# Kernel optimization log

Measured on AMD Instinct MI355X. Metric: run time of the kernel, lower is better.

Reference implementation:

```python
import jax, jax.numpy as jnp
import numpy as np

N_IN, N_REC, T, BATCH = 128, 512, 1000, 64
ALPHA = 0.2
SIGMA = float(np.sqrt(2.0 / ALPHA) * 0.05)  # sqrt(2/alpha)*sigma_rec
EI_RATIO = 0.8
W_REC_GAIN = 1.0


def setup_inputs() -> dict:
    key = jax.random.key(0)
    k_x, k_n = jax.random.split(key)
    rng = np.random.RandomState(0)
    # w_in init: randn/sqrt(n_in)
    w_in = (rng.randn(N_IN, N_REC) / np.sqrt(N_IN)).astype(np.float32)
    # w_rec init 'randgauss' with Dale's law: abs, inhibitory rows scaled
    n_ex = int(N_REC * EI_RATIO)
    w_rec0 = W_REC_GAIN * rng.randn(N_REC, N_REC) / np.sqrt(N_REC)
    w_rec0 = np.abs(w_rec0)
    w_rec0[n_ex:, :] *= EI_RATIO / (1.0 - EI_RATIO)
    w_rec = w_rec0.astype(np.float32)
    ei_vec = np.concatenate([np.ones(n_ex), -np.ones(N_REC - n_ex)]).astype(np.float32)
    ei_mask = np.diag(ei_vec)
    autapse_mask = np.ones((N_REC, N_REC), dtype=np.float32)
    np.fill_diagonal(autapse_mask, 0.0)
    x = jax.random.normal(k_x, (BATCH, T, N_IN), dtype=jnp.float32)
    # pre-scaled noise: randn * sigma, one draw per timestep (matches torch.randn_like(h)*sigma)
    noise = jax.random.normal(k_n, (BATCH, T, N_REC), dtype=jnp.float32) * SIGMA
    return {
        "x": x,
        "w_in": jnp.asarray(w_in),
        "w_rec": jnp.asarray(w_rec),
        "b_rec": jnp.zeros((N_REC,), dtype=jnp.float32),
        "ei_mask": jnp.asarray(ei_mask),
        "autapse_mask": jnp.asarray(autapse_mask),
        "noise": noise,
    }


def reference(x, w_in, w_rec, b_rec, ei_mask, autapse_mask, noise):
    # Effective recurrent weight, computed ONCE (torch code recomputes each step)
    w_eff = ei_mask @ (w_rec * autapse_mask)          # (n_rec, n_rec)
    inp_all = jnp.einsum("bti,ir->btr", x, w_in)       # precompute input projection
    xs = (jnp.swapaxes(inp_all, 0, 1), jnp.swapaxes(noise, 0, 1))  # (T,b,r)
    h0 = jnp.zeros((x.shape[0], w_rec.shape[0]), dtype=x.dtype)

    def step(h, xt):
        inp_t, noise_t = xt
        pre = inp_t + h @ w_eff + b_rec + noise_t
        h_new = (1.0 - ALPHA) * h + ALPHA * jax.nn.relu(pre)
        return h_new, h_new

    _, h_all = jax.lax.scan(step, h0, xs)              # (T, batch, n_rec)
    return jnp.swapaxes(h_all, 0, 1)                   # (batch, T, n_rec)
```

## Files before the change

### kernel.cpp

```cpp
#include <hip/hip_runtime.h>

#define T_STEPS 1000
#define NIN     128
#define NREC    512
#define NBATCH  64
#define ALPHA   0.2f

#define NSLICE  4
#define SCOLS   128
#define NGRP    8
#define KPER    64

#define WS_W_OFF     0
#define WS_COMM_OFF  (1u << 20)
#define COMM_U64     (NBATCH * NREC)
#define WS_NEEDED    (WS_COMM_OFF + 2 * COMM_U64 * 8)

#define LDS_BARRIER() do {                                        \
    asm volatile("s_waitcnt lgkmcnt(0)" ::: "memory");            \
    __builtin_amdgcn_s_barrier();                                 \
    asm volatile("" ::: "memory");                                \
} while (0)

__global__ void weff_kernel(const float* __restrict__ w_rec,
                            const float* __restrict__ ei_mask,
                            const float* __restrict__ autapse,
                            float* __restrict__ w_eff) {
    int idx = blockIdx.x * blockDim.x + threadIdx.x;
    if (idx < NREC * NREC) {
        int row = idx >> 9;
        float ei = ei_mask[row * NREC + row];
        w_eff[idx] = ei * w_rec[idx] * autapse[idx];
    }
}

__global__ __launch_bounds__(1024) void gemm_in_kernel(
        const float* __restrict__ x,
        const float* __restrict__ w_in,
        const float* __restrict__ b_rec,
        float* __restrict__ io) {
    __shared__ float xs[32][NIN];

    const int tid = threadIdx.x;
    const int m0  = blockIdx.x * 32;

    {
        const float4* src = reinterpret_cast<const float4*>(x + (size_t)m0 * NIN);
        reinterpret_cast<float4*>(&xs[0][0])[tid] = src[tid];
    }
    __syncthreads();

    const int j0 = tid & 255;
    const int j1 = j0 + 256;
    const int rg = tid >> 8;

    float acc[8][2];
#pragma unroll
    for (int i = 0; i < 8; ++i) { acc[i][0] = 0.f; acc[i][1] = 0.f; }

#pragma unroll 4
    for (int k = 0; k < NIN; ++k) {
        float wv0 = w_in[k * NREC + j0];
        float wv1 = w_in[k * NREC + j1];
#pragma unroll
        for (int i = 0; i < 8; ++i) {
            float xv = xs[rg * 8 + i][k];
            acc[i][0] = fmaf(xv, wv0, acc[i][0]);
            acc[i][1] = fmaf(xv, wv1, acc[i][1]);
        }
    }

    const float br0 = b_rec[j0];
    const float br1 = b_rec[j1];
#pragma unroll
    for (int i = 0; i < 8; ++i) {
        size_t ro = (size_t)(m0 + rg * 8 + i) * NREC;
        io[ro + j0] = acc[i][0] + br0;
        io[ro + j1] = acc[i][1] + br1;
    }
}

__global__ __launch_bounds__(1024, 4) void rnn_coop(
        const float* __restrict__ W,
        const float* __restrict__ noise,
        float* __restrict__ io,
        unsigned long long* __restrict__ comm) {
    __shared__ __align__(16) float h_lds[NREC];
    __shared__ float part[NGRP * SCOLS];

    const int tid = threadIdx.x;
    const int b   = blockIdx.x >> 2;
    const int s   = blockIdx.x & 3;
    const int jl  = tid & (SCOLS - 1);
    const int g   = tid >> 7;
    const int ln  = tid & 63;
    const int jg  = s * SCOLS + jl;
    const bool remote = (g >> 1) != s;
    const int cslot = g * KPER + ln;

    float Wr[KPER];
    {
        const float* wp = W + (size_t)(g * KPER) * NREC + jg;
#pragma unroll
        for (int u = 0; u < KPER; ++u)
            Wr[u] = wp[(size_t)u * NREC];
    }
#pragma unroll
    for (int u = 0; u < KPER; ++u)
        asm volatile("" : "+v"(Wr[u]));

    if (tid < NREC) h_lds[tid] = 0.f;
    __syncthreads();

    float hj = 0.f;
    const size_t iobase = (size_t)b * T_STEPS * NREC + jg;
    const unsigned long long* cbase = comm + (size_t)b * NREC + cslot;
    unsigned long long* cwbase = comm + (size_t)b * NREC + jg;

    float inp = 0.f, nz = 0.f;
    if (tid < SCOLS) { inp = io[iobase]; nz = noise[iobase]; }

    for (int t = 0; t < T_STEPS; ++t) {
        const size_t off = iobase + (size_t)t * NREC;

        float inp_n = 0.f, nz_n = 0.f;
        if (t + 1 < T_STEPS && tid < SCOLS) {
            inp_n = io[off + NREC];
            nz_n  = noise[off + NREC];
        }

        if (t > 0 && remote) {
            const unsigned long long* cp = cbase + (size_t)(t & 1) * COMM_U64;
            unsigned long long v = __hip_atomic_load(
                cp, __ATOMIC_RELAXED, __HIP_MEMORY_SCOPE_AGENT);
            while ((int)(unsigned)(v >> 32) < t)
                v = __hip_atomic_load(cp, __ATOMIC_RELAXED,
                                      __HIP_MEMORY_SCOPE_AGENT);
            asm volatile("" ::: "memory");
            h_lds[cslot] = __uint_as_float((unsigned)(v & 0xffffffffu));
        }

        float a0 = 0.f, a1 = 0.f, a2 = 0.f, a3 = 0.f;
        const float4* h4 = reinterpret_cast<const float4*>(&h_lds[g * KPER]);
#pragma unroll
        for (int u = 0; u < KPER / 4; ++u) {
            float4 hv = h4[u];
            a0 = fmaf(hv.x, Wr[4 * u + 0], a0);
            a1 = fmaf(hv.y, Wr[4 * u + 1], a1);
            a2 = fmaf(hv.z, Wr[4 * u + 2], a2);
            a3 = fmaf(hv.w, Wr[4 * u + 3], a3);
        }
        part[g * SCOLS + jl] = (a0 + a1) + (a2 + a3);
        LDS_BARRIER();

        if (tid < SCOLS) {
            float pre = inp + nz;
#pragma unroll
            for (int q = 0; q < NGRP; ++q)
                pre += part[q * SCOLS + jl];
            float hnew = (1.f - ALPHA) * hj + ALPHA * fmaxf(pre, 0.f);
            hj = hnew;
            h_lds[jg] = hnew;
            unsigned long long pv =
                ((unsigned long long)(unsigned)(t + 1) << 32) |
                (unsigned long long)__float_as_uint(hnew);
            __hip_atomic_store(cwbase + (size_t)((t + 1) & 1) * COMM_U64, pv,
                               __ATOMIC_RELAXED, __HIP_MEMORY_SCOPE_AGENT);
            io[off] = hnew;
        }
        inp = inp_n; nz = nz_n;
        LDS_BARRIER();
    }
}

__global__ __launch_bounds__(1024) void rnn_kernel(
        const float* __restrict__ W,
        const float* __restrict__ noise,
        float* __restrict__ io) {
    __shared__ float h[NREC];
    __shared__ float part2[NREC];

    const int tid  = threadIdx.x;
    const int j    = tid & (NREC - 1);
    const int half = tid >> 9;
    const int b    = blockIdx.x;

    if (tid < NREC) h[tid] = 0.f;
    float hj = 0.f;
    __syncthreads();

    const int kb = half * 256;
    const float* wp = W + (size_t)kb * NREC + j;
    const size_t base = (size_t)b * T_STEPS * NREC + j;

    for (int t = 0; t < T_STEPS; ++t) {
        const size_t off = base + (size_t)t * NREC;
        float acc = (half == 0) ? (io[off] + noise[off]) : 0.f;
#pragma unroll
        for (int ku = 0; ku < 256; ku += 16) {
            float w[16];
#pragma unroll
            for (int u = 0; u < 16; ++u) w[u] = wp[(size_t)(ku + u) * NREC];
#pragma unroll
            for (int u = 0; u < 16; ++u) acc = fmaf(h[kb + ku + u], w[u], acc);
        }
        if (half == 1) part2[j] = acc;
        __syncthreads();
        if (half == 0) {
            float pre  = acc + part2[j];
            float hnew = (1.f - ALPHA) * hj + ALPHA * fmaxf(pre, 0.f);
            io[off] = hnew;
            h[j] = hnew;
            hj = hnew;
        }
        __syncthreads();
    }
}

extern "C" void kernel_launch(void* const* d_in, const int* in_sizes, int n_in,
                              void* d_out, int out_size, void* d_ws, size_t ws_size,
                              hipStream_t stream) {
    const float* x       = (const float*)d_in[0];
    const float* w_in    = (const float*)d_in[1];
    const float* w_rec   = (const float*)d_in[2];
    const float* b_rec   = (const float*)d_in[3];
    const float* ei_mask = (const float*)d_in[4];
    const float* autapse = (const float*)d_in[5];
    const float* noise   = (const float*)d_in[6];
    float* out = (float*)d_out;

    char* ws = (char*)d_ws;
    float* W = (float*)(ws + WS_W_OFF);
    unsigned long long* comm = (unsigned long long*)(ws + WS_COMM_OFF);

    weff_kernel<<<dim3((NREC * NREC + 255) / 256), dim3(256), 0, stream>>>(
        w_rec, ei_mask, autapse, W);

    gemm_in_kernel<<<dim3(64000 / 32), dim3(1024), 0, stream>>>(
        x, w_in, b_rec, out);

    if (ws_size >= (size_t)WS_NEEDED) {
        hipMemsetAsync(comm, 0, 2 * COMM_U64 * 8, stream);
        void* args[] = {(void*)&W, (void*)&noise, (void*)&out, (void*)&comm};
        hipLaunchCooperativeKernel(reinterpret_cast<void*>(rnn_coop),
                                   dim3(NBATCH * NSLICE), dim3(1024),
                                   args, 0, stream);
    } else {
        rnn_kernel<<<dim3(NBATCH), dim3(1024), 0, stream>>>(W, noise, out);
    }
}
```

Baseline: 1.675 ms.

## Add L2-local communication path and remap blocks so batch slices share an XCD

Blocks are remapped so that the four slices of one batch element have block IDs 8 apart, which under round-robin XCD dispatch should land them on the same XCD and its shared L2. Each h value is now written twice: once with a plain L2 store to a second comm buffer, and once with the existing agent-scope atomic. Readers poll the L2 copy with sc0 loads and fall back to the LLC copy on each retry. The aim is lower inter-block handoff latency per timestep, but correctness relies on an assumed block-to-XCD placement, and the extra store adds traffic.

```diff
diff --git a/kernel.cpp b/kernel.cpp
--- a/kernel.cpp
+++ b/kernel.cpp
@@ -11,16 +11,41 @@
 #define NGRP    8
 #define KPER    64
 
-#define WS_W_OFF     0
-#define WS_COMM_OFF  (1u << 20)
-#define COMM_U64     (NBATCH * NREC)
-#define WS_NEEDED    (WS_COMM_OFF + 2 * COMM_U64 * 8)
+#define WS_W_OFF      0
+#define WS_COMM_OFF   (1u << 20)
+#define COMM_U64      (NBATCH * NREC)
+#define COMM_BYTES    (2 * COMM_U64 * 8)
+#define WS_COMM2_OFF  (WS_COMM_OFF + COMM_BYTES)
+#define WS_NEEDED_LLC (WS_COMM_OFF + COMM_BYTES)
+#define WS_NEEDED_DUAL (WS_COMM2_OFF + COMM_BYTES)
 
 #define LDS_BARRIER() do {                                        \
     asm volatile("s_waitcnt lgkmcnt(0)" ::: "memory");            \
     __builtin_amdgcn_s_barrier();                                 \
     asm volatile("" ::: "memory");                                \
 } while (0)
+
+__device__ __forceinline__ unsigned long long ld_l2(
+        const unsigned long long* p) {
+    unsigned long long r;
+    asm volatile("global_load_dwordx2 %0, %1, off sc0\n\t"
+                 "s_waitcnt vmcnt(0)"
+                 : "=v"(r) : "v"(p) : "memory");
+    return r;
+}
+__device__ __forceinline__ void st_l2(unsigned long long* p,
+                                      unsigned long long v) {
+    asm volatile("global_store_dwordx2 %0, %1, off"
+                 :: "v"(p), "v"(v) : "memory");
+}
+__device__ __forceinline__ unsigned long long ld_llc(
+        const unsigned long long* p) {
+    return __hip_atomic_load(p, __ATOMIC_RELAXED, __HIP_MEMORY_SCOPE_AGENT);
+}
+__device__ __forceinline__ void st_llc(unsigned long long* p,
+                                       unsigned long long v) {
+    __hip_atomic_store(p, v, __ATOMIC_RELAXED, __HIP_MEMORY_SCOPE_AGENT);
+}
 
 __global__ void weff_kernel(const float* __restrict__ w_rec,
                             const float* __restrict__ ei_mask,
@@ -84,19 +109,22 @@
         const float* __restrict__ W,
         const float* __restrict__ noise,
         float* __restrict__ io,
-        unsigned long long* __restrict__ comm) {
+        unsigned long long* __restrict__ comm,
+        unsigned long long* __restrict__ comm2) {
     __shared__ __align__(16) float h_lds[NREC];
     __shared__ float part[NGRP * SCOLS];
 
     const int tid = threadIdx.x;
-    const int b   = blockIdx.x >> 2;
-    const int s   = blockIdx.x & 3;
+    const int bid = blockIdx.x;
+    const int b   = (bid & 7) + 8 * (bid >> 5);
+    const int s   = (bid >> 3) & 3;
     const int jl  = tid & (SCOLS - 1);
     const int g   = tid >> 7;
     const int ln  = tid & 63;
     const int jg  = s * SCOLS + jl;
     const bool remote = (g >> 1) != s;
     const int cslot = g * KPER + ln;
+    const bool use_l2 = (comm2 != nullptr);
 
     float Wr[KPER];
     {
@@ -114,8 +142,10 @@
 
     float hj = 0.f;
     const size_t iobase = (size_t)b * T_STEPS * NREC + jg;
-    const unsigned long long* cbase = comm + (size_t)b * NREC + cslot;
-    unsigned long long* cwbase = comm + (size_t)b * NREC + jg;
+    const unsigned long long* cbase  = comm  + (size_t)b * NREC + cslot;
+    const unsigned long long* cbase2 = comm2 + (size_t)b * NREC + cslot;
+    unsigned long long* cwr  = comm  + (size_t)b * NREC + jg;
+    unsigned long long* cwr2 = comm2 + (size_t)b * NREC + jg;
 
     float inp = 0.f, nz = 0.f;
     if (tid < SCOLS) { inp = io[iobase]; nz = noise[iobase]; }
@@ -130,12 +160,20 @@
         }
 
         if (t > 0 && remote) {
-            const unsigned long long* cp = cbase + (size_t)(t & 1) * COMM_U64;
-            unsigned long long v = __hip_atomic_load(
-                cp, __ATOMIC_RELAXED, __HIP_MEMORY_SCOPE_AGENT);
-            while ((int)(unsigned)(v >> 32) < t)
-                v = __hip_atomic_load(cp, __ATOMIC_RELAXED,
-                                      __HIP_MEMORY_SCOPE_AGENT);
+            const size_t po = (size_t)(t & 1) * COMM_U64;
+            unsigned long long v;
+            if (use_l2) {
+                v = ld_l2(cbase2 + po);
+                while ((int)(unsigned)(v >> 32) < t) {
+                    v = ld_llc(cbase + po);
+                    if ((int)(unsigned)(v >> 32) >= t) break;
+                    v = ld_l2(cbase2 + po);
+                }
+            } else {
+                v = ld_llc(cbase + po);
+                while ((int)(unsigned)(v >> 32) < t)
+                    v = ld_llc(cbase + po);
+            }
             asm volatile("" ::: "memory");
             h_lds[cslot] = __uint_as_float((unsigned)(v & 0xffffffffu));
         }
@@ -164,8 +202,9 @@
             unsigned long long pv =
                 ((unsigned long long)(unsigned)(t + 1) << 32) |
                 (unsigned long long)__float_as_uint(hnew);
-            __hip_atomic_store(cwbase + (size_t)((t + 1) & 1) * COMM_U64, pv,
-                               __ATOMIC_RELAXED, __HIP_MEMORY_SCOPE_AGENT);
+            const size_t po = (size_t)((t + 1) & 1) * COMM_U64;
+            if (use_l2) st_l2(cwr2 + po, pv);
+            st_llc(cwr + po, pv);
             io[off] = hnew;
         }
         inp = inp_n; nz = nz_n;
@@ -231,7 +270,8 @@
 
     char* ws = (char*)d_ws;
     float* W = (float*)(ws + WS_W_OFF);
-    unsigned long long* comm = (unsigned long long*)(ws + WS_COMM_OFF);
+    unsigned long long* comm  = (unsigned long long*)(ws + WS_COMM_OFF);
+    unsigned long long* comm2 = (unsigned long long*)(ws + WS_COMM2_OFF);
 
     weff_kernel<<<dim3((NREC * NREC + 255) / 256), dim3(256), 0, stream>>>(
         w_rec, ei_mask, autapse, W);
@@ -239,9 +279,18 @@
     gemm_in_kernel<<<dim3(64000 / 32), dim3(1024), 0, stream>>>(
         x, w_in, b_rec, out);
 
-    if (ws_size >= (size_t)WS_NEEDED) {
-        hipMemsetAsync(comm, 0, 2 * COMM_U64 * 8, stream);
-        void* args[] = {(void*)&W, (void*)&noise, (void*)&out, (void*)&comm};
+    if (ws_size >= (size_t)WS_NEEDED_DUAL) {
+        hipMemsetAsync(comm, 0, 2 * COMM_BYTES, stream);
+        void* args[] = {(void*)&W, (void*)&noise, (void*)&out,
+                        (void*)&comm, (void*)&comm2};
+        hipLaunchCooperativeKernel(reinterpret_cast<void*>(rnn_coop),
+                                   dim3(NBATCH * NSLICE), dim3(1024),
+                                   args, 0, stream);
+    } else if (ws_size >= (size_t)WS_NEEDED_LLC) {
+        hipMemsetAsync(comm, 0, COMM_BYTES, stream);
+        unsigned long long* nul = nullptr;
+        void* args[] = {(void*)&W, (void*)&noise, (void*)&out,
+                        (void*)&comm, (void*)&nul};
         hipLaunchCooperativeKernel(reinterpret_cast<void*>(rnn_coop),
                                    dim3(NBATCH * NSLICE), dim3(1024),
                                    args, 0, stream);
```

Result: slower. 1.754 ms (+4.7%).
